# Kernel optimization log

Hardware: AMD Instinct MI355X
Metric: run time of the kernel (lower is better)

## Reference

```python
import jax, jax.numpy as jnp
import numpy as np

B, C, L = 8, 2048, 256          # batch, seq (EEG channels), feature length
E = 3 * L                        # embed_dim = 768 (fused QKV width)
H = 4                            # attention heads
D = E // (3 * H)                 # head_dim = 64
SCALE = 8.0                      # hardcoded in the module (== sqrt(D) here)


def _layer_norm(x, gamma, beta, eps=1e-5):
    mu = jnp.mean(x, axis=-1, keepdims=True)
    var = jnp.var(x, axis=-1, keepdims=True)
    return (x - mu) * jax.lax.rsqrt(var + eps) * gamma + beta


def setup_inputs() -> dict:
    key = jax.random.key(0)
    ks = jax.random.split(key, 5)
    x = jax.random.normal(ks[0], (B, C, L), dtype=jnp.float32)
    # layers_1: Linear(L -> E) + LayerNorm(E)
    W1 = jax.random.normal(ks[1], (L, E), dtype=jnp.float32) / np.sqrt(L)
    b1 = jnp.zeros((E,), dtype=jnp.float32)
    g1 = jnp.ones((E,), dtype=jnp.float32)
    beta1 = jnp.zeros((E,), dtype=jnp.float32)
    # layers_2: Linear(L -> L) + LayerNorm(L)
    W2 = jax.random.normal(ks[2], (L, L), dtype=jnp.float32) / np.sqrt(L)
    b2 = jnp.zeros((L,), dtype=jnp.float32)
    g2 = jnp.ones((L,), dtype=jnp.float32)
    beta2 = jnp.zeros((L,), dtype=jnp.float32)
    return {"x": x, "W1": W1, "b1": b1, "g1": g1, "beta1": beta1,
            "W2": W2, "b2": b2, "g2": g2, "beta2": beta2}


def reference(x, W1, b1, g1, beta1, W2, b2, g2, beta2):
    b, c, _ = x.shape
    # layers_1 (dropout is identity in eval mode)
    y = _layer_norm(x @ W1 + b1, g1, beta1)                     # [b, c, E]
    qkv = y.reshape(b, c, 3, H, D).transpose(2, 0, 3, 1, 4)     # [3, b, H, c, D]
    q, k, v = qkv[0], qkv[1], qkv[2]
    attn = jax.nn.softmax(jnp.einsum('bhqd,bhkd->bhqk', q, k) / SCALE, axis=-1)
    o = jnp.einsum('bhqk,bhkd->bhqd', attn, v)                  # [b, H, c, D]
    o = o.transpose(0, 2, 1, 3).reshape(b, c, H * D)            # [b, c, L]
    # layers_2 + residual
    z = _layer_norm(o @ W2 + b2, g2, beta2) + x
    return z
```

## Files before the change

### kernel.cpp

```cpp
#include <hip/hip_runtime.h>
#include <hip/hip_bf16.h>

#define B_ 8
#define C_ 2048
#define L_ 256
#define E_ 768
#define H_ 4
#define D_ 64
#define M_ (B_*C_)

typedef __attribute__((ext_vector_type(8))) short short8v;
typedef __attribute__((ext_vector_type(4))) short short4v;
typedef __attribute__((ext_vector_type(4))) float f32x4;
typedef __attribute__((ext_vector_type(4))) unsigned uint4v;

__device__ __forceinline__ short f2bf(float f) {
  union { float f; unsigned u; } v; v.f = f;
  unsigned r = v.u + 0x7FFFu + ((v.u >> 16) & 1u);
  return (short)(r >> 16);
}
__device__ __forceinline__ unsigned cvtpk(float a, float b) {
  unsigned r;
  asm("v_cvt_pk_bf16_f32 %0, %1, %2" : "=v"(r) : "v"(a), "v"(b));
  return r;
}
__device__ __forceinline__ float exp2x(float x) {
  float r;
  asm("v_exp_f32 %0, %1" : "=v"(r) : "v"(x));
  return r;
}

__device__ __forceinline__ void gll16(const void* g, void* l) {
  __builtin_amdgcn_global_load_lds(
      (const __attribute__((address_space(1))) unsigned int*)g,
      (__attribute__((address_space(3))) unsigned int*)l, 16, 0, 0);
}

__global__ __launch_bounds__(256) void transpose_w_kernel(
    const float* __restrict__ W1, short* __restrict__ W1t,
    const float* __restrict__ W2, short* __restrict__ W2t) {
  __shared__ float ld[32][33];
  const int isW1 = blockIdx.y < 24;
  const float* W = isW1 ? W1 : W2;
  short* Wt = isW1 ? W1t : W2t;
  const int N = isW1 ? E_ : L_;
  const int k0 = blockIdx.x * 32, n0 = (isW1 ? blockIdx.y : blockIdx.y - 24) * 32;
  const int tx = threadIdx.x & 31, ty = threadIdx.x >> 5;
  #pragma unroll
  for (int j = 0; j < 4; ++j)
    ld[ty + j*8][tx] = W[(size_t)(k0 + ty + j*8) * N + n0 + tx];
  __syncthreads();
  const int r  = threadIdx.x >> 3;
  const int c0 = (threadIdx.x & 7) * 4;
  short4v o;
  o[0]=f2bf(ld[c0+0][r]); o[1]=f2bf(ld[c0+1][r]);
  o[2]=f2bf(ld[c0+2][r]); o[3]=f2bf(ld[c0+3][r]);
  *(short4v*)(Wt + (size_t)(n0 + r) * 256 + k0 + c0) = o;
}

__global__ __launch_bounds__(512, 2) void gemm1_ln_fused_kernel(
    const float* __restrict__ x, const short* __restrict__ W1t,
    const float* __restrict__ b1, const float* __restrict__ g1,
    const float* __restrict__ be1,
    short* __restrict__ Qg, short* __restrict__ Kg, short* __restrict__ Vtg) {
  __shared__ short As[64*264];
  __shared__ short Bs[2][24576];
  __shared__ short tbuf[8][64][24];
  __shared__ float2 red[8][64];
  __shared__ float mu_s[64], rs_s[64];
  const int tid = threadIdx.x;
  const int w = tid >> 6, l = tid & 63, lo = l & 15, hi = l >> 4;
  const int m0 = blockIdx.x * 64;
  const int b = m0 >> 11, c0 = m0 & (C_ - 1);
  const int nbase = w * 96;

  #pragma unroll
  for (int half = 0; half < 2; ++half) {
    const int row = (tid >> 4) + half * 32, cc = (tid & 15) * 16;
    const float* ap = x + (size_t)(m0 + row) * 256 + cc;
    float4 a0 = ((const float4*)ap)[0], a1 = ((const float4*)ap)[1];
    float4 a2 = ((const float4*)ap)[2], a3 = ((const float4*)ap)[3];
    uint4 p0, p1;
    p0.x = cvtpk(a0.x,a0.y); p0.y = cvtpk(a0.z,a0.w);
    p0.z = cvtpk(a1.x,a1.y); p0.w = cvtpk(a1.z,a1.w);
    p1.x = cvtpk(a2.x,a2.y); p1.y = cvtpk(a2.z,a2.w);
    p1.z = cvtpk(a3.x,a3.y); p1.w = cvtpk(a3.z,a3.w);
    *(uint4*)&As[row*264 + cc]     = p0;
    *(uint4*)&As[row*264 + cc + 8] = p1;
  }

  f32x4 acc[4][6];
  #pragma unroll
  for (int m = 0; m < 4; ++m)
    #pragma unroll
    for (int n = 0; n < 6; ++n) acc[m][n] = (f32x4){0.f,0.f,0.f,0.f};

  const int srowl = l >> 2;
  const int schunk = ((l & 3) ^ (srowl & 3)) << 3;

  #pragma unroll
  for (int i = 0; i < 6; ++i) {
    const short* src = W1t + (size_t)(i*128 + w*16 + srowl) * 256 + schunk;
    gll16(src, &Bs[0][i*4096 + w*512]);
  }
  __syncthreads();

  for (int r8 = 0; r8 < 8; ++r8) {
    if (r8) __builtin_amdgcn_s_barrier();
    if (r8 < 7) {
      #pragma unroll
      for (int i = 0; i < 6; ++i) {
        const short* src = W1t + (size_t)(i*128 + w*16 + srowl) * 256
                         + (r8+1)*32 + schunk;
        gll16(src, &Bs[(r8+1)&1][i*4096 + w*512]);
      }
      asm volatile("s_waitcnt vmcnt(6)" ::: "memory");
    } else {
      asm volatile("s_waitcnt vmcnt(0)" ::: "memory");
    }
    __builtin_amdgcn_s_barrier();
    const short* Bc = &Bs[r8&1][0];

    short8v af[4];
    #pragma unroll
    for (int m = 0; m < 4; ++m)
      af[m] = *(short8v*)&As[(m*16 + lo)*264 + r8*32 + hi*8];
    #pragma unroll
    for (int n = 0; n < 6; ++n) {
      const int row = nbase + n*16 + lo;
      short8v bfn = *(const short8v*)&Bc[row*32 + ((hi ^ (lo & 3)) << 3)];
      #pragma unroll
      for (int m = 0; m < 4; ++m)
        acc[m][n] = __builtin_amdgcn_mfma_f32_16x16x32_bf16(af[m], bfn, acc[m][n], 0,0,0);
    }
  }

  float bb[6], ggv[6], eev[6];
  #pragma unroll
  for (int n = 0; n < 6; ++n) {
    int col = nbase + n*16 + lo;
    bb[n] = b1[col]; ggv[n] = g1[col]; eev[n] = be1[col];
  }
  #pragma unroll
  for (int m = 0; m < 4; ++m)
    #pragma unroll
    for (int r = 0; r < 4; ++r) {
      float s = 0.f, s2 = 0.f;
      #pragma unroll
      for (int n = 0; n < 6; ++n) {
        float v = acc[m][n][r] + bb[n];
        acc[m][n][r] = v;
        s += v; s2 += v*v;
      }
      #pragma unroll
      for (int off = 1; off < 16; off <<= 1) {
        s  += __shfl_xor(s, off);
        s2 += __shfl_xor(s2, off);
      }
      if (lo == 0) red[w][m*16 + hi*4 + r] = make_float2(s, s2);
    }
  __syncthreads();
  if (tid < 64) {
    float s = 0.f, s2 = 0.f;
    #pragma unroll
    for (int wv = 0; wv < 8; ++wv) { s += red[wv][tid].x; s2 += red[wv][tid].y; }
    float mu = s * (1.f / E_);
    float var = s2 * (1.f / E_) - mu * mu;
    mu_s[tid] = mu;
    rs_s[tid] = rsqrtf(var + 1e-5f);
  }
  __syncthreads();

  const float qs = 0.18033688011f;
  float muv[4][4], rsv[4][4];
  #pragma unroll
  for (int m = 0; m < 4; ++m)
    #pragma unroll
    for (int r = 0; r < 4; ++r) {
      int row = m*16 + hi*4 + r;
      muv[m][r] = mu_s[row]; rsv[m][r] = rs_s[row];
    }

  #pragma unroll
  for (int n = 0; n < 6; ++n) {
    const int e0b = nbase + n*16;
    if (e0b < 512) {
      const float qscale = (e0b < 256) ? qs : 1.f;
      #pragma unroll
      for (int m = 0; m < 4; ++m)
        #pragma unroll
        for (int r = 0; r < 4; ++r) {
          float v = (acc[m][n][r] - muv[m][r]) * rsv[m][r] * ggv[n] + eev[n];
          tbuf[w][m*16 + hi*4 + r][lo] = f2bf(v * qscale);
        }
      #pragma unroll
      for (int half = 0; half < 2; ++half) {
        const int trow = (l >> 1) + half * 32, tc = (l & 1) * 8;
        short8v tv = *(short8v*)&tbuf[w][trow][tc];
        const int c = c0 + trow;
        if (e0b < 256) {
          const int h = e0b >> 6, d0 = (e0b & 63) + tc;
          *(short8v*)(Qg + ((size_t)(b*H_ + h) * C_ + c) * D_ + d0) = tv;
        } else {
          const int eb = e0b - 256, h = eb >> 6, d0 = (eb & 63) + tc;
          int a5 = c & 31;
          int p5 = (((a5 >> 2) & 1) << 4) | (((a5 >> 3) & 3) << 2) | (a5 & 3);
          int cs = (c & ~31) | p5;
          *(short8v*)(Kg + ((size_t)(b*H_ + h) * C_ + cs) * D_
                        + (((d0 >> 3) ^ (cs & 7)) << 3)) = tv;
        }
      }
    } else {
      const int e0 = e0b + lo;
      const int eb = e0 - 512, h = eb >> 6, d = eb & 63;
      #pragma unroll
      for (int m = 0; m < 4; ++m) {
        short4v pk;
        #pragma unroll
        for (int r = 0; r < 4; ++r)
          pk[r] = f2bf((acc[m][n][r] - muv[m][r]) * rsv[m][r] * ggv[n] + eev[n]);
        const int c = c0 + m*16 + hi*4;
        size_t off = ((size_t)(b*H_ + h) * D_ + d) * C_ + (c & ~63)
                   + ((((c & 63) >> 3) ^ (d & 7)) << 3) + (c & 7);
        *(short4v*)(Vtg + off) = pk;
      }
    }
  }
}

__global__ __launch_bounds__(256, 3) void attn_mfma_kernel(
    const short* __restrict__ Qg, const short* __restrict__ Kg,
    const short* __restrict__ Vtg, short* __restrict__ ob) {
  __shared__ short Ks[3][4096];
  __shared__ short Vs[3][4096];
  const int tid = threadIdx.x;
  const int w  = tid >> 6;
  const int l  = tid & 63, lo = l & 15, hi = l >> 4;
  const int sw = lo & 7;
  const int bh = blockIdx.x, qt = blockIdx.y;
  const size_t hd = (size_t)bh * (C_ * D_);
  const int q0 = qt * 128 + w * 32;

  const short8v bqA0 = *(const short8v*)(Qg + hd + (size_t)(q0+lo)*D_ + hi*8);
  const short8v bqA1 = *(const short8v*)(Qg + hd + (size_t)(q0+lo)*D_ + 32 + hi*8);
  const short8v bqB0 = *(const short8v*)(Qg + hd + (size_t)(q0+16+lo)*D_ + hi*8);
  const short8v bqB1 = *(const short8v*)(Qg + hd + (size_t)(q0+16+lo)*D_ + 32 + hi*8);

  short8v ones;
  #pragma unroll
  for (int j = 0; j < 8; ++j) ones[j] = (short)0x3F80;

  const short* Ktile = Kg + hd;
  const short* Vrow  = Vtg + hd;
  const int segA = w*2, segB = segA + 1;
  const int kOffA = segA*512 + l*8, kOffB = segB*512 + l*8;
  const size_t vOffA = (size_t)(segA*8 + (l>>3)) * C_ + (l&7)*8;
  const size_t vOffB = (size_t)(segB*8 + (l>>3)) * C_ + (l&7)*8;

  f32x4 OaccA[4] = {{0,0,0,0},{0,0,0,0},{0,0,0,0},{0,0,0,0}};
  f32x4 OaccB[4] = {{0,0,0,0},{0,0,0,0},{0,0,0,0},{0,0,0,0}};
  f32x4 LaccA = {0.f,0.f,0.f,0.f}, LaccB = {0.f,0.f,0.f,0.f};
  const f32x4 zero4 = {0.f, 0.f, 0.f, 0.f};

  gll16(Ktile + kOffA, &Ks[0][segA*512]);
  gll16(Ktile + kOffB, &Ks[0][segB*512]);
  gll16(Vrow + vOffA,  &Vs[0][segA*512]);
  gll16(Vrow + vOffB,  &Vs[0][segB*512]);

  int cur = 0, nxt = 1;
  for (int kt = 0; kt < 32; ++kt) {
    asm volatile("s_waitcnt vmcnt(0)" ::: "memory");
    __builtin_amdgcn_s_barrier();
    if (kt != 31) {
      const short* kn = Ktile + (size_t)(kt+1) * 4096;
      const short* vn = Vrow  + (size_t)(kt+1) * 64;
      gll16(kn + kOffA, &Ks[nxt][segA*512]);
      gll16(kn + kOffB, &Ks[nxt][segB*512]);
      gll16(vn + vOffA, &Vs[nxt][segA*512]);
      gll16(vn + vOffB, &Vs[nxt][segB*512]);
    }
    const short* Kc = &Ks[cur][0];
    const short* Vc = &Vs[cur][0];

    f32x4 stA[4], stB[4];
    __builtin_amdgcn_s_setprio(1);
    #pragma unroll
    for (int mt = 0; mt < 4; ++mt) {
      short8v ka = *(const short8v*)&Kc[(mt*16 + lo)*64 + ((hi ^ sw) << 3)];
      short8v kb = *(const short8v*)&Kc[(mt*16 + lo)*64 + (((4 + hi) ^ sw) << 3)];
      f32x4 zA = __builtin_amdgcn_mfma_f32_16x16x32_bf16(ka, bqA0, zero4, 0, 0, 0);
      stA[mt]  = __builtin_amdgcn_mfma_f32_16x16x32_bf16(kb, bqA1, zA, 0, 0, 0);
      f32x4 zB = __builtin_amdgcn_mfma_f32_16x16x32_bf16(ka, bqB0, zero4, 0, 0, 0);
      stB[mt]  = __builtin_amdgcn_mfma_f32_16x16x32_bf16(kb, bqB1, zB, 0, 0, 0);
    }
    __builtin_amdgcn_s_setprio(0);

    float psA[16], psB[16];
    #pragma unroll
    for (int mt = 0; mt < 4; ++mt)
      #pragma unroll
      for (int r = 0; r < 4; ++r) {
        psA[mt*4 + r] = exp2x(stA[mt][r]);
        psB[mt*4 + r] = exp2x(stB[mt][r]);
      }
    uint4v uA0 = { cvtpk(psA[0], psA[1]),  cvtpk(psA[2], psA[3]),
                   cvtpk(psA[4], psA[5]),  cvtpk(psA[6], psA[7]) };
    uint4v uA1 = { cvtpk(psA[8], psA[9]),  cvtpk(psA[10], psA[11]),
                   cvtpk(psA[12], psA[13]), cvtpk(psA[14], psA[15]) };
    uint4v uB0 = { cvtpk(psB[0], psB[1]),  cvtpk(psB[2], psB[3]),
                   cvtpk(psB[4], psB[5]),  cvtpk(psB[6], psB[7]) };
    uint4v uB1 = { cvtpk(psB[8], psB[9]),  cvtpk(psB[10], psB[11]),
                   cvtpk(psB[12], psB[13]), cvtpk(psB[14], psB[15]) };
    short8v paA0 = __builtin_bit_cast(short8v, uA0);
    short8v paA1 = __builtin_bit_cast(short8v, uA1);
    short8v paB0 = __builtin_bit_cast(short8v, uB0);
    short8v paB1 = __builtin_bit_cast(short8v, uB1);

    __builtin_amdgcn_s_setprio(1);
    LaccA = __builtin_amdgcn_mfma_f32_16x16x32_bf16(paA0, ones, LaccA, 0, 0, 0);
    LaccA = __builtin_amdgcn_mfma_f32_16x16x32_bf16(paA1, ones, LaccA, 0, 0, 0);
    LaccB = __builtin_amdgcn_mfma_f32_16x16x32_bf16(paB0, ones, LaccB, 0, 0, 0);
    LaccB = __builtin_amdgcn_mfma_f32_16x16x32_bf16(paB1, ones, LaccB, 0, 0, 0);
    #pragma unroll
    for (int nt = 0; nt < 4; ++nt) {
      short8v vb0 = *(const short8v*)&Vc[(nt*16 + lo)*64 + ((hi ^ sw) << 3)];
      short8v vb1 = *(const short8v*)&Vc[(nt*16 + lo)*64 + (((4 + hi) ^ sw) << 3)];
      OaccA[nt] = __builtin_amdgcn_mfma_f32_16x16x32_bf16(paA0, vb0, OaccA[nt], 0,0,0);
      OaccA[nt] = __builtin_amdgcn_mfma_f32_16x16x32_bf16(paA1, vb1, OaccA[nt], 0,0,0);
      OaccB[nt] = __builtin_amdgcn_mfma_f32_16x16x32_bf16(paB0, vb0, OaccB[nt], 0,0,0);
      OaccB[nt] = __builtin_amdgcn_mfma_f32_16x16x32_bf16(paB1, vb1, OaccB[nt], 0,0,0);
    }
    __builtin_amdgcn_s_setprio(0);
    cur = nxt;
    nxt = (nxt == 2) ? 0 : nxt + 1;
  }

  float invA[4], invB[4];
  #pragma unroll
  for (int r = 0; r < 4; ++r) { invA[r] = 1.f / LaccA[r]; invB[r] = 1.f / LaccB[r]; }
  const int b = bh >> 2, h = bh & 3;
  short* obpA = ob + ((size_t)b * C_ + q0) * L_ + h * D_;
  short* obpB = ob + ((size_t)b * C_ + q0 + 16) * L_ + h * D_;
  #pragma unroll
  for (int nt = 0; nt < 4; ++nt)
    #pragma unroll
    for (int r = 0; r < 4; ++r) {
      obpA[(hi*4 + r) * L_ + nt*16 + lo] = f2bf(OaccA[nt][r] * invA[r]);
      obpB[(hi*4 + r) * L_ + nt*16 + lo] = f2bf(OaccB[nt][r] * invB[r]);
    }
}

__global__ __launch_bounds__(256, 4) void gemm2_ln_mfma_kernel(
    const short* __restrict__ ob, const short* __restrict__ W2t,
    const float* __restrict__ b2, const float* __restrict__ g2,
    const float* __restrict__ be2, const float* __restrict__ x,
    float* __restrict__ out) {
  __shared__ short As[32*264];
  __shared__ float2 red[4][32];
  __shared__ float mu_s[32], rs_s[32];
  const int tid = threadIdx.x;
  const int w = tid >> 6, l = tid & 63, lo = l & 15, hi = l >> 4;
  const int m0 = blockIdx.x * 32;
  const int nbase = w * 64;

  #pragma unroll
  for (int i = 0; i < 4; ++i) {
    int id = tid + i * 256;
    int row = id >> 5, c8 = (id & 31) * 8;
    *(short8v*)&As[row*264 + c8] =
        *(const short8v*)(ob + (size_t)(m0 + row) * 256 + c8);
  }
  __syncthreads();

  f32x4 acc[2][4];
  #pragma unroll
  for (int m = 0; m < 2; ++m)
    #pragma unroll
    for (int n = 0; n < 4; ++n) acc[m][n] = (f32x4){0.f,0.f,0.f,0.f};

  #pragma unroll
  for (int kt = 0; kt < 4; ++kt)
    #pragma unroll
    for (int kk = 0; kk < 2; ++kk) {
      short8v bf[4];
      #pragma unroll
      for (int n = 0; n < 4; ++n)
        bf[n] = *(const short8v*)(W2t + (size_t)(nbase + n*16 + lo) * 256
                                     + kt*64 + kk*32 + hi*8);
      short8v af0 = *(short8v*)&As[lo*264      + kt*64 + kk*32 + hi*8];
      short8v af1 = *(short8v*)&As[(16+lo)*264 + kt*64 + kk*32 + hi*8];
      #pragma unroll
      for (int n = 0; n < 4; ++n) {
        acc[0][n] = __builtin_amdgcn_mfma_f32_16x16x32_bf16(af0, bf[n], acc[0][n], 0,0,0);
        acc[1][n] = __builtin_amdgcn_mfma_f32_16x16x32_bf16(af1, bf[n], acc[1][n], 0,0,0);
      }
    }

  float bb[4], gg[4], ee[4];
  #pragma unroll
  for (int n = 0; n < 4; ++n) {
    int col = nbase + n*16 + lo;
    bb[n] = b2[col]; gg[n] = g2[col]; ee[n] = be2[col];
  }
  #pragma unroll
  for (int m = 0; m < 2; ++m)
    #pragma unroll
    for (int r = 0; r < 4; ++r) {
      float s = 0.f, s2 = 0.f;
      #pragma unroll
      for (int n = 0; n < 4; ++n) {
        float v = acc[m][n][r] + bb[n];
        acc[m][n][r] = v;
        s += v; s2 += v*v;
      }
      #pragma unroll
      for (int off = 1; off < 16; off <<= 1) {
        s  += __shfl_xor(s, off);
        s2 += __shfl_xor(s2, off);
      }
      if (lo == 0) red[w][m*16 + hi*4 + r] = make_float2(s, s2);
    }
  __syncthreads();
  if (tid < 32) {
    float s = 0.f, s2 = 0.f;
    #pragma unroll
    for (int wv = 0; wv < 4; ++wv) { s += red[wv][tid].x; s2 += red[wv][tid].y; }
    float mu = s * (1.f / L_);
    float var = s2 * (1.f / L_) - mu * mu;
    mu_s[tid] = mu;
    rs_s[tid] = rsqrtf(var + 1e-5f);
  }
  __syncthreads();

  #pragma unroll
  for (int m = 0; m < 2; ++m) {
    float mu4[4], rs4[4];
    #pragma unroll
    for (int r = 0; r < 4; ++r) {
      int row = m*16 + hi*4 + r;
      mu4[r] = mu_s[row]; rs4[r] = rs_s[row];
    }
    #pragma unroll
    for (int r = 0; r < 4; ++r) {
      const int grow = m0 + m*16 + hi*4 + r;
      const float* xr = x + (size_t)grow * L_ + nbase;
      float* orow = out + (size_t)grow * L_ + nbase;
      #pragma unroll
      for (int n = 0; n < 4; ++n)
        orow[n*16 + lo] = (acc[m][n][r] - mu4[r]) * rs4[r] * gg[n] + ee[n]
                        + xr[n*16 + lo];
    }
  }
}

extern "C" void kernel_launch(void* const* d_in, const int* in_sizes, int n_in,
                              void* d_out, int out_size, void* d_ws, size_t ws_size,
                              hipStream_t stream) {
  const float* x   = (const float*)d_in[0];
  const float* W1  = (const float*)d_in[1];
  const float* b1  = (const float*)d_in[2];
  const float* g1  = (const float*)d_in[3];
  const float* be1 = (const float*)d_in[4];
  const float* W2  = (const float*)d_in[5];
  const float* b2  = (const float*)d_in[6];
  const float* g2  = (const float*)d_in[7];
  const float* be2 = (const float*)d_in[8];
  float* out = (float*)d_out;

  const size_t HDSZ = (size_t)B_ * H_ * C_ * D_;
  short* W1t = (short*)d_ws;
  short* W2t = W1t + (size_t)L_ * E_;
  short* Qg  = W2t + (size_t)L_ * L_;
  short* Kg  = Qg  + HDSZ;
  short* Vtg = Kg  + HDSZ;
  short* obm = Vtg + HDSZ;

  transpose_w_kernel<<<dim3(8, 32), 256, 0, stream>>>(W1, W1t, W2, W2t);
  gemm1_ln_fused_kernel<<<M_ / 64, 512, 0, stream>>>(x, W1t, b1, g1, be1, Qg, Kg, Vtg);
  attn_mfma_kernel<<<dim3(32, C_ / 128), 256, 0, stream>>>(Qg, Kg, Vtg, obm);
  gemm2_ln_mfma_kernel<<<M_ / 32, 256, 0, stream>>>(obm, W2t, b2, g2, be2, x, out);
}
```

Before: 87.36 us.

## Split attention over key range into two partial passes, combine in GEMM2 prologue

The attention kernel now runs two blocks per query tile, each covering half of the key sequence, and writes unnormalized partial outputs in bf16 plus row sums to workspace. The GEMM2 kernel sums the two partials and divides by the combined sum when it loads its A tile. The LDS ring drops from triple to double buffering, with a reordered waitcnt/barrier scheme, and launch bounds rise to 4 blocks per CU for more parallelism and occupancy. The cost is extra global traffic for the doubled partial output and an extra rounding of the partials to bf16. The split is only correct without a running max because softmax here is computed without max subtraction.

```diff
diff --git a/kernel.cpp b/kernel.cpp
--- a/kernel.cpp
+++ b/kernel.cpp
@@ -18,6 +18,10 @@
   union { float f; unsigned u; } v; v.f = f;
   unsigned r = v.u + 0x7FFFu + ((v.u >> 16) & 1u);
   return (short)(r >> 16);
+}
+__device__ __forceinline__ float bf2f(short s) {
+  union { unsigned u; float f; } v; v.u = ((unsigned)(unsigned short)s) << 16;
+  return v.f;
 }
 __device__ __forceinline__ unsigned cvtpk(float a, float b) {
   unsigned r;
@@ -228,18 +232,20 @@
   }
 }
 
-__global__ __launch_bounds__(256, 3) void attn_mfma_kernel(
+__global__ __launch_bounds__(256, 4) void attn_mfma_kernel(
     const short* __restrict__ Qg, const short* __restrict__ Kg,
-    const short* __restrict__ Vtg, short* __restrict__ ob) {
-  __shared__ short Ks[3][4096];
-  __shared__ short Vs[3][4096];
+    const short* __restrict__ Vtg, short* __restrict__ obm,
+    float* __restrict__ lg) {
+  __shared__ short Ks[2][4096];
+  __shared__ short Vs[2][4096];
   const int tid = threadIdx.x;
   const int w  = tid >> 6;
   const int l  = tid & 63, lo = l & 15, hi = l >> 4;
   const int sw = lo & 7;
-  const int bh = blockIdx.x, qt = blockIdx.y;
+  const int bh = blockIdx.x, qt = blockIdx.y, ks = blockIdx.z;
   const size_t hd = (size_t)bh * (C_ * D_);
   const int q0 = qt * 128 + w * 32;
+  const int kt0 = ks * 16;
 
   const short8v bqA0 = *(const short8v*)(Qg + hd + (size_t)(q0+lo)*D_ + hi*8);
   const short8v bqA1 = *(const short8v*)(Qg + hd + (size_t)(q0+lo)*D_ + 32 + hi*8);
@@ -250,8 +256,8 @@
   #pragma unroll
   for (int j = 0; j < 8; ++j) ones[j] = (short)0x3F80;
 
-  const short* Ktile = Kg + hd;
-  const short* Vrow  = Vtg + hd;
+  const short* Ktile = Kg + hd + (size_t)kt0 * 4096;
+  const short* Vrow  = Vtg + hd + (size_t)kt0 * 64;
   const int segA = w*2, segB = segA + 1;
   const int kOffA = segA*512 + l*8, kOffB = segB*512 + l*8;
   const size_t vOffA = (size_t)(segA*8 + (l>>3)) * C_ + (l&7)*8;
@@ -267,18 +273,21 @@
   gll16(Vrow + vOffA,  &Vs[0][segA*512]);
   gll16(Vrow + vOffB,  &Vs[0][segB*512]);
 
-  int cur = 0, nxt = 1;
-  for (int kt = 0; kt < 32; ++kt) {
-    asm volatile("s_waitcnt vmcnt(0)" ::: "memory");
+  int cur = 0;
+  for (int ktl = 0; ktl < 16; ++ktl) {
     __builtin_amdgcn_s_barrier();
-    if (kt != 31) {
-      const short* kn = Ktile + (size_t)(kt+1) * 4096;
-      const short* vn = Vrow  + (size_t)(kt+1) * 64;
-      gll16(kn + kOffA, &Ks[nxt][segA*512]);
-      gll16(kn + kOffB, &Ks[nxt][segB*512]);
-      gll16(vn + vOffA, &Vs[nxt][segA*512]);
-      gll16(vn + vOffB, &Vs[nxt][segB*512]);
-    }
+    if (ktl != 15) {
+      const short* kn = Ktile + (size_t)(ktl+1) * 4096;
+      const short* vn = Vrow  + (size_t)(ktl+1) * 64;
+      gll16(kn + kOffA, &Ks[cur^1][segA*512]);
+      gll16(kn + kOffB, &Ks[cur^1][segB*512]);
+      gll16(vn + vOffA, &Vs[cur^1][segA*512]);
+      gll16(vn + vOffB, &Vs[cur^1][segB*512]);
+      asm volatile("s_waitcnt vmcnt(4)" ::: "memory");
+    } else {
+      asm volatile("s_waitcnt vmcnt(0)" ::: "memory");
+    }
+    __builtin_amdgcn_s_barrier();
     const short* Kc = &Ks[cur][0];
     const short* Vc = &Vs[cur][0];
 
@@ -331,27 +340,32 @@
       OaccB[nt] = __builtin_amdgcn_mfma_f32_16x16x32_bf16(paB1, vb1, OaccB[nt], 0,0,0);
     }
     __builtin_amdgcn_s_setprio(0);
-    cur = nxt;
-    nxt = (nxt == 2) ? 0 : nxt + 1;
-  }
-
-  float invA[4], invB[4];
-  #pragma unroll
-  for (int r = 0; r < 4; ++r) { invA[r] = 1.f / LaccA[r]; invB[r] = 1.f / LaccB[r]; }
+    cur ^= 1;
+  }
+
   const int b = bh >> 2, h = bh & 3;
-  short* obpA = ob + ((size_t)b * C_ + q0) * L_ + h * D_;
-  short* obpB = ob + ((size_t)b * C_ + q0 + 16) * L_ + h * D_;
+  short* obpA = obm + (size_t)ks * (M_ * L_) + ((size_t)b * C_ + q0) * L_ + h * D_;
+  short* obpB = obpA + (size_t)16 * L_;
   #pragma unroll
   for (int nt = 0; nt < 4; ++nt)
     #pragma unroll
     for (int r = 0; r < 4; ++r) {
-      obpA[(hi*4 + r) * L_ + nt*16 + lo] = f2bf(OaccA[nt][r] * invA[r]);
-      obpB[(hi*4 + r) * L_ + nt*16 + lo] = f2bf(OaccB[nt][r] * invB[r]);
-    }
+      obpA[(hi*4 + r) * L_ + nt*16 + lo] = f2bf(OaccA[nt][r]);
+      obpB[(hi*4 + r) * L_ + nt*16 + lo] = f2bf(OaccB[nt][r]);
+    }
+  if (lo == 0) {
+    float* lp = lg + ((size_t)ks * 32 + bh) * C_ + q0;
+    #pragma unroll
+    for (int r = 0; r < 4; ++r) {
+      lp[hi*4 + r]      = LaccA[r];
+      lp[16 + hi*4 + r] = LaccB[r];
+    }
+  }
 }
 
 __global__ __launch_bounds__(256, 4) void gemm2_ln_mfma_kernel(
-    const short* __restrict__ ob, const short* __restrict__ W2t,
+    const short* __restrict__ obm, const float* __restrict__ lg,
+    const short* __restrict__ W2t,
     const float* __restrict__ b2, const float* __restrict__ g2,
     const float* __restrict__ be2, const float* __restrict__ x,
     float* __restrict__ out) {
@@ -361,14 +375,25 @@
   const int tid = threadIdx.x;
   const int w = tid >> 6, l = tid & 63, lo = l & 15, hi = l >> 4;
   const int m0 = blockIdx.x * 32;
+  const int bb_ = m0 >> 11, cb = m0 & (C_ - 1);
   const int nbase = w * 64;
 
   #pragma unroll
   for (int i = 0; i < 4; ++i) {
     int id = tid + i * 256;
     int row = id >> 5, c8 = (id & 31) * 8;
-    *(short8v*)&As[row*264 + c8] =
-        *(const short8v*)(ob + (size_t)(m0 + row) * 256 + c8);
+    int h = c8 >> 6;
+    size_t goff = (size_t)(m0 + row) * 256 + c8;
+    short8v o1 = *(const short8v*)(obm + goff);
+    short8v o2 = *(const short8v*)(obm + (size_t)(M_ * L_) + goff);
+    float l1 = lg[(size_t)(bb_*4 + h) * C_ + cb + row];
+    float l2 = lg[(size_t)(32 + bb_*4 + h) * C_ + cb + row];
+    float inv = 1.f / (l1 + l2);
+    short8v o;
+    #pragma unroll
+    for (int j = 0; j < 8; ++j)
+      o[j] = f2bf((bf2f(o1[j]) + bf2f(o2[j])) * inv);
+    *(short8v*)&As[row*264 + c8] = o;
   }
   __syncthreads();
 
@@ -474,9 +499,10 @@
   short* Kg  = Qg  + HDSZ;
   short* Vtg = Kg  + HDSZ;
   short* obm = Vtg + HDSZ;
+  float* lg  = (float*)(obm + 2 * (size_t)M_ * L_);
 
   transpose_w_kernel<<<dim3(8, 32), 256, 0, stream>>>(W1, W1t, W2, W2t);
   gemm1_ln_fused_kernel<<<M_ / 64, 512, 0, stream>>>(x, W1t, b1, g1, be1, Qg, Kg, Vtg);
-  attn_mfma_kernel<<<dim3(32, C_ / 128), 256, 0, stream>>>(Qg, Kg, Vtg, obm);
-  gemm2_ln_mfma_kernel<<<M_ / 32, 256, 0, stream>>>(obm, W2t, b2, g2, be2, x, out);
-}
+  attn_mfma_kernel<<<dim3(32, C_ / 128, 2), 256, 0, stream>>>(Qg, Kg, Vtg, obm, lg);
+  gemm2_ln_mfma_kernel<<<M_ / 32, 256, 0, stream>>>(obm, lg, W2t, b2, g2, be2, x, out);
+}
```

New measurement: 86.73 us. About the same (-0.7%).
